# Kernel optimization log

Measured on AMD Instinct MI355X. Metric: run time of the kernel, lower is better.

The kernel has to match this reference:

```python
import jax, jax.numpy as jnp
import numpy as np
from jax import lax

EMB = 128  # embed_length
R = 4      # CBAM reduction


def _mlp(v, w1, b1, w2, b2):
    # shared CAM MLP: [B,C] -> [B,C//r] -> [B,C]
    return jax.nn.relu(v @ w1.T + b1) @ w2.T + b2


def _cbam(x, w1, b1, w2, b2, sw):
    # channel attention (CAM)
    mx = jnp.max(x, axis=(2, 3))
    av = jnp.mean(x, axis=(2, 3))
    gate = jax.nn.sigmoid(_mlp(mx, w1, b1, w2, b2) + _mlp(av, w1, b1, w2, b2))
    y = gate[:, :, None, None] * x
    # spatial attention (SAM): 7x7 conv over [max, mean] channel maps
    smx = jnp.max(y, axis=1, keepdims=True)
    sav = jnp.mean(y, axis=1, keepdims=True)
    s = lax.conv_general_dilated(jnp.concatenate([smx, sav], axis=1), sw,
                                 window_strides=(1, 1), padding=[(3, 3), (3, 3)])
    y = jax.nn.sigmoid(s) * y
    return y + x  # residual as in CBAM.forward


def _neck(x, w, b):
    # 1x1 conv == channel GEMM
    return jnp.einsum('bchw,oc->bohw', x, w) + b[None, :, None, None]


def setup_inputs() -> dict:
    key = jax.random.key(0)
    ks = jax.random.split(key, 40)
    B = 32
    f32 = jnp.float32
    inp = {
        'xin0': jax.random.normal(ks[0], (B, 256, 80, 80), f32),
        'xin1': jax.random.normal(ks[1], (B, 512, 40, 40), f32),
        'xin2': jax.random.normal(ks[2], (B, 1024, 20, 20), f32),
        'yolo_outputs': jax.random.normal(ks[3], (B, 8400, 6), f32),
        'reid_idx': jax.random.randint(ks[4], (B, 100), 0, 8400, dtype=jnp.int32),
        # 1x1 neck convs
        'nw0': jax.random.normal(ks[5], (EMB, 256), f32) * 0.05,
        'nb0': jnp.zeros((EMB,), f32),
        'nw1': jax.random.normal(ks[6], (EMB, 512), f32) * 0.05,
        'nb1': jnp.zeros((EMB,), f32),
        'nw2': jax.random.normal(ks[7], (EMB, 1024), f32) * 0.05,
        'nb2': jnp.zeros((EMB,), f32),
    }
    h = EMB // R
    for i in range(3):
        k = jax.random.split(ks[10 + i], 5)
        inp[f'c{i}w1'] = jax.random.normal(k[0], (h, EMB), f32) * 0.05
        inp[f'c{i}b1'] = jnp.zeros((h,), f32)
        inp[f'c{i}w2'] = jax.random.normal(k[1], (EMB, h), f32) * 0.05
        inp[f'c{i}b2'] = jnp.zeros((EMB,), f32)
        inp[f'c{i}sw'] = jax.random.normal(k[2], (1, 2, 7, 7), f32) * 0.05
    return inp


def reference(xin0, xin1, xin2, yolo_outputs, reid_idx,
              nw0, nb0, nw1, nb1, nw2, nb2,
              c0w1, c0b1, c0w2, c0b2, c0sw,
              c1w1, c1b1, c1w2, c1b2, c1sw,
              c2w1, c2b1, c2w2, c2b2, c2sw):
    f0 = _cbam(_neck(xin0, nw0, nb0), c0w1, c0b1, c0w2, c0b2, c0sw)
    f1 = _cbam(_neck(xin1, nw1, nb1), c1w1, c1b1, c1w2, c1b2, c1sw)
    f2 = _cbam(_neck(xin2, nw2, nb2), c2w1, c2b1, c2w2, c2b2, c2sw)
    B, C = f0.shape[0], f0.shape[1]
    reid_feat = jnp.concatenate([f0.reshape(B, C, -1),
                                 f1.reshape(B, C, -1),
                                 f2.reshape(B, C, -1)], axis=2)  # [B, C, 8400]
    # ragged per-batch gather reid_feat[b, :, reid_idx[b]] then stack columns -> [B*K, C]
    emb = jax.vmap(lambda f, idx: f[:, idx].T)(reid_feat, reid_idx)  # [B, K, C]
    return (yolo_outputs, emb.reshape(-1, C))
```

## Files before the change

### kernel.cpp

```cpp
#include <hip/hip_runtime.h>
#include <hip/hip_bf16.h>

typedef __attribute__((ext_vector_type(8))) short bf16x8;
typedef __attribute__((ext_vector_type(4))) float f32x4;

#define EMB 128
#define NB 32

__device__ __forceinline__ unsigned short f2bf(float f) {
  unsigned u = __float_as_uint(f);
  u = u + 0x7FFFu + ((u >> 16) & 1u);
  return (unsigned short)(u >> 16);
}
__device__ __forceinline__ unsigned ordf(float f) {
  unsigned u = __float_as_uint(f);
  return (u & 0x80000000u) ? ~u : (u | 0x80000000u);
}
__device__ __forceinline__ float unordf(unsigned v) {
  unsigned u = (v & 0x80000000u) ? (v & 0x7FFFFFFFu) : ~v;
  return __uint_as_float(u);
}

__global__ __launch_bounds__(256) void neck_kernel(
    const float* __restrict__ x, const float* __restrict__ w, const float* __restrict__ bias,
    unsigned short* __restrict__ f, unsigned* __restrict__ gmax, float* __restrict__ gsum,
    int K, int HW)
{
  __shared__ unsigned smax[EMB];
  __shared__ float ssum[EMB];
  const int tid = threadIdx.x;
  if (tid < EMB) { smax[tid] = 0u; ssum[tid] = 0.f; }
  __syncthreads();

  const int wv = tid >> 6, lane = tid & 63, q = lane >> 4, col = lane & 15;
  const int b = blockIdx.y;
  const int p0 = blockIdx.x * 128 + wv * 32;
  const float* __restrict__ xb = x + (size_t)b * K * HW;

  f32x4 acc[2][8];
#pragma unroll
  for (int mt = 0; mt < 2; mt++)
#pragma unroll
    for (int nt = 0; nt < 8; nt++) acc[mt][nt] = (f32x4){0.f, 0.f, 0.f, 0.f};

  const int pm0 = min(p0 + col, HW - 1);
  const int pm1 = min(p0 + 16 + col, HW - 1);

  for (int c0 = 0; c0 < K; c0 += 32) {
    const int cb = c0 + q * 8;
    float a0[8], a1[8];
#pragma unroll
    for (int j = 0; j < 8; j++) {
      const float* row = xb + (size_t)(cb + j) * HW;
      a0[j] = row[pm0];
      a1[j] = row[pm1];
    }
    bf16x8 A0, A1;
#pragma unroll
    for (int j = 0; j < 8; j++) { A0[j] = (short)f2bf(a0[j]); A1[j] = (short)f2bf(a1[j]); }
#pragma unroll
    for (int nt = 0; nt < 8; nt++) {
      const float* wr = w + (size_t)(nt * 16 + col) * K + cb;
      const float4 wa = *(const float4*)(wr);
      const float4 wb = *(const float4*)(wr + 4);
      bf16x8 Bf;
      Bf[0] = (short)f2bf(wa.x); Bf[1] = (short)f2bf(wa.y);
      Bf[2] = (short)f2bf(wa.z); Bf[3] = (short)f2bf(wa.w);
      Bf[4] = (short)f2bf(wb.x); Bf[5] = (short)f2bf(wb.y);
      Bf[6] = (short)f2bf(wb.z); Bf[7] = (short)f2bf(wb.w);
      acc[0][nt] = __builtin_amdgcn_mfma_f32_16x16x32_bf16(A0, Bf, acc[0][nt], 0, 0, 0);
      acc[1][nt] = __builtin_amdgcn_mfma_f32_16x16x32_bf16(A1, Bf, acc[1][nt], 0, 0, 0);
    }
  }

#pragma unroll
  for (int nt = 0; nt < 8; nt++) {
    const int o = nt * 16 + col;
    const float bo = bias[o];
    float lmax = -3.4e38f, lsum = 0.f;
#pragma unroll
    for (int mt = 0; mt < 2; mt++) {
#pragma unroll
      for (int r = 0; r < 4; r++) {
        const int p = p0 + mt * 16 + q * 4 + r;
        const float v = acc[mt][nt][r] + bo;
        if (p < HW) {
          f[((size_t)b * HW + p) * EMB + o] = f2bf(v);
          lmax = fmaxf(lmax, v);
          lsum += v;
        }
      }
    }
#pragma unroll
    for (int off = 16; off < 64; off <<= 1) {
      lmax = fmaxf(lmax, __shfl_xor(lmax, off, 64));
      lsum += __shfl_xor(lsum, off, 64);
    }
    if (lane < 16) {
      atomicMax(&smax[o], ordf(lmax));
      atomicAdd(&ssum[o], lsum);
    }
  }
  __syncthreads();
  if (tid < EMB) {
    atomicMax(&gmax[b * EMB + tid], smax[tid]);
    atomicAdd(&gsum[b * EMB + tid], ssum[tid]);
  }
}

__global__ __launch_bounds__(128) void gate_kernel(
    const unsigned* __restrict__ gmax, const float* __restrict__ gsum, float* __restrict__ gate,
    const float* __restrict__ w1a, const float* __restrict__ b1a, const float* __restrict__ w2a, const float* __restrict__ b2a,
    const float* __restrict__ w1b, const float* __restrict__ b1b, const float* __restrict__ w2b, const float* __restrict__ b2b,
    const float* __restrict__ w1c, const float* __restrict__ b1c, const float* __restrict__ w2c, const float* __restrict__ b2c)
{
  const int s = blockIdx.y, b = blockIdx.x, tid = threadIdx.x;
  const float* w1 = s == 0 ? w1a : (s == 1 ? w1b : w1c);
  const float* b1 = s == 0 ? b1a : (s == 1 ? b1b : b1c);
  const float* w2 = s == 0 ? w2a : (s == 1 ? w2b : w2c);
  const float* b2 = s == 0 ? b2a : (s == 1 ? b2b : b2c);
  const float invHW = s == 0 ? (1.f / 6400.f) : (s == 1 ? (1.f / 1600.f) : (1.f / 400.f));
  __shared__ float mx[EMB], av[EMB], hm[32], ha[32];
  const int base = (s * NB + b) * EMB;
  mx[tid] = unordf(gmax[base + tid]);
  av[tid] = gsum[base + tid] * invHW;
  __syncthreads();
  if (tid < 32) {
    float sm = b1[tid], sa = b1[tid];
    for (int c = 0; c < EMB; c++) { const float wv = w1[tid * EMB + c]; sm += wv * mx[c]; sa += wv * av[c]; }
    hm[tid] = fmaxf(sm, 0.f); ha[tid] = fmaxf(sa, 0.f);
  }
  __syncthreads();
  float v = 2.f * b2[tid];
  for (int h = 0; h < 32; h++) { const float wv = w2[tid * 32 + h]; v += wv * (hm[h] + ha[h]); }
  gate[base + tid] = 1.f / (1.f + __expf(-v));
}

__global__ __launch_bounds__(256) void smap_kernel(
    const unsigned short* __restrict__ f0, const unsigned short* __restrict__ f1, const unsigned short* __restrict__ f2,
    const float* __restrict__ gate,
    float* __restrict__ smx0, float* __restrict__ sav0,
    float* __restrict__ smx1, float* __restrict__ sav1,
    float* __restrict__ smx2, float* __restrict__ sav2)
{
  const int lane = threadIdx.x & 63;
  const int wid = (blockIdx.x * blockDim.x + threadIdx.x) >> 6;
  const int nw = (gridDim.x * blockDim.x) >> 6;
  const int total = NB * 8400;
  for (int t = wid; t < total; t += nw) {
    const int b = t / 8400, p = t % 8400;
    const unsigned short* f; float* smx; float* sav; int s, pp, HW;
    if (p < 6400)      { s = 0; pp = p;        HW = 6400; f = f0; smx = smx0; sav = sav0; }
    else if (p < 8000) { s = 1; pp = p - 6400; HW = 1600; f = f1; smx = smx1; sav = sav1; }
    else               { s = 2; pp = p - 8000; HW = 400;  f = f2; smx = smx2; sav = sav2; }
    const unsigned u = ((const unsigned*)(f + ((size_t)b * HW + pp) * EMB))[lane];
    const float v0 = __uint_as_float(u << 16);
    const float v1 = __uint_as_float(u & 0xFFFF0000u);
    const int gb = (s * NB + b) * EMB + 2 * lane;
    const float y0 = gate[gb] * v0, y1 = gate[gb + 1] * v1;
    float m = fmaxf(y0, y1), sm = y0 + y1;
#pragma unroll
    for (int off = 1; off < 64; off <<= 1) { m = fmaxf(m, __shfl_xor(m, off, 64)); sm += __shfl_xor(sm, off, 64); }
    if (lane == 0) { smx[b * HW + pp] = m; sav[b * HW + pp] = sm * (1.f / EMB); }
  }
}

__global__ __launch_bounds__(256) void gather_kernel(
    const int* __restrict__ reid_idx,
    const unsigned short* __restrict__ f0, const unsigned short* __restrict__ f1, const unsigned short* __restrict__ f2,
    const float* __restrict__ gate,
    const float* __restrict__ smx0, const float* __restrict__ sav0,
    const float* __restrict__ smx1, const float* __restrict__ sav1,
    const float* __restrict__ smx2, const float* __restrict__ sav2,
    const float* __restrict__ sw0, const float* __restrict__ sw1, const float* __restrict__ sw2,
    float* __restrict__ emb)
{
  const int lane = threadIdx.x & 63;
  const int wid = (blockIdx.x * blockDim.x + threadIdx.x) >> 6;
  if (wid >= NB * 100) return;
  const int b = wid / 100, k = wid % 100;
  const int idx = reid_idx[b * 100 + k];
  const unsigned short* f; const float* smx; const float* sav; const float* sw;
  int s, pp, W, H, HW;
  if (idx < 6400)      { s = 0; pp = idx;        W = 80; H = 80; HW = 6400; f = f0; smx = smx0; sav = sav0; sw = sw0; }
  else if (idx < 8000) { s = 1; pp = idx - 6400; W = 40; H = 40; HW = 1600; f = f1; smx = smx1; sav = sav1; sw = sw1; }
  else                 { s = 2; pp = idx - 8000; W = 20; H = 20; HW = 400;  f = f2; smx = smx2; sav = sav2; sw = sw2; }
  const int y = pp / W, xx0 = pp % W;
  float c = 0.f;
  if (lane < 49) {
    const int dy = lane / 7 - 3, dx = lane % 7 - 3;
    const int yy = y + dy, xx = xx0 + dx;
    if (yy >= 0 && yy < H && xx >= 0 && xx < W) {
      const int qq = b * HW + yy * W + xx;
      c = smx[qq] * sw[lane] + sav[qq] * sw[49 + lane];
    }
  }
#pragma unroll
  for (int off = 1; off < 64; off <<= 1) c += __shfl_xor(c, off, 64);
  const float sig = 1.f / (1.f + __expf(-c));
  const unsigned u = ((const unsigned*)(f + ((size_t)b * HW + pp) * EMB))[lane];
  const float v0 = __uint_as_float(u << 16);
  const float v1 = __uint_as_float(u & 0xFFFF0000u);
  const int gb = (s * NB + b) * EMB + 2 * lane;
  const float o0 = v0 * (1.f + sig * gate[gb]);
  const float o1 = v1 * (1.f + sig * gate[gb + 1]);
  *(float2*)(emb + ((size_t)(b * 100 + k)) * EMB + 2 * lane) = make_float2(o0, o1);
}

extern "C" void kernel_launch(void* const* d_in, const int* in_sizes, int n_in,
                              void* d_out, int out_size, void* d_ws, size_t ws_size,
                              hipStream_t stream)
{
  const float* xin0 = (const float*)d_in[0];
  const float* xin1 = (const float*)d_in[1];
  const float* xin2 = (const float*)d_in[2];
  const float* yolo = (const float*)d_in[3];
  const int*   reid = (const int*)d_in[4];
  const float* nw0 = (const float*)d_in[5];  const float* nb0 = (const float*)d_in[6];
  const float* nw1 = (const float*)d_in[7];  const float* nb1 = (const float*)d_in[8];
  const float* nw2 = (const float*)d_in[9];  const float* nb2 = (const float*)d_in[10];
  const float* c0w1 = (const float*)d_in[11]; const float* c0b1 = (const float*)d_in[12];
  const float* c0w2 = (const float*)d_in[13]; const float* c0b2 = (const float*)d_in[14];
  const float* c0sw = (const float*)d_in[15];
  const float* c1w1 = (const float*)d_in[16]; const float* c1b1 = (const float*)d_in[17];
  const float* c1w2 = (const float*)d_in[18]; const float* c1b2 = (const float*)d_in[19];
  const float* c1sw = (const float*)d_in[20];
  const float* c2w1 = (const float*)d_in[21]; const float* c2b1 = (const float*)d_in[22];
  const float* c2w2 = (const float*)d_in[23]; const float* c2b2 = (const float*)d_in[24];
  const float* c2sw = (const float*)d_in[25];

  char* ws = (char*)d_ws;
  size_t off = 0;
  auto alloc = [&](size_t bytes) -> void* {
    void* p = ws + off; off += (bytes + 255) & ~(size_t)255; return p;
  };
  unsigned short* f0 = (unsigned short*)alloc((size_t)NB * 6400 * EMB * 2);
  unsigned short* f1 = (unsigned short*)alloc((size_t)NB * 1600 * EMB * 2);
  unsigned short* f2 = (unsigned short*)alloc((size_t)NB * 400 * EMB * 2);
  unsigned* gmax = (unsigned*)alloc(3 * NB * EMB * 4);
  float* gsum = (float*)alloc(3 * NB * EMB * 4);
  float* gate = (float*)alloc(3 * NB * EMB * 4);
  float* smx0 = (float*)alloc((size_t)NB * 6400 * 4);
  float* sav0 = (float*)alloc((size_t)NB * 6400 * 4);
  float* smx1 = (float*)alloc((size_t)NB * 1600 * 4);
  float* sav1 = (float*)alloc((size_t)NB * 1600 * 4);
  float* smx2 = (float*)alloc((size_t)NB * 400 * 4);
  float* sav2 = (float*)alloc((size_t)NB * 400 * 4);

  hipMemsetAsync(gmax, 0, (size_t)2 * 3 * NB * EMB * 4, stream);
  hipMemcpyAsync(d_out, yolo, (size_t)NB * 8400 * 6 * 4, hipMemcpyDeviceToDevice, stream);

  dim3 blk(256);
  neck_kernel<<<dim3(50, NB), blk, 0, stream>>>(xin0, nw0, nb0, f0, gmax + 0 * NB * EMB, gsum + 0 * NB * EMB, 256, 6400);
  neck_kernel<<<dim3(13, NB), blk, 0, stream>>>(xin1, nw1, nb1, f1, gmax + 1 * NB * EMB, gsum + 1 * NB * EMB, 512, 1600);
  neck_kernel<<<dim3(4,  NB), blk, 0, stream>>>(xin2, nw2, nb2, f2, gmax + 2 * NB * EMB, gsum + 2 * NB * EMB, 1024, 400);

  gate_kernel<<<dim3(NB, 3), dim3(128), 0, stream>>>(gmax, gsum, gate,
      c0w1, c0b1, c0w2, c0b2, c1w1, c1b1, c1w2, c1b2, c2w1, c2b1, c2w2, c2b2);

  smap_kernel<<<dim3(4200), blk, 0, stream>>>(f0, f1, f2, gate, smx0, sav0, smx1, sav1, smx2, sav2);

  gather_kernel<<<dim3(800), blk, 0, stream>>>(reid, f0, f1, f2, gate,
      smx0, sav0, smx1, sav1, smx2, sav2, c0sw, c1sw, c2sw,
      (float*)d_out + (size_t)NB * 8400 * 6);
}
```

Before: 710.0 us.

## Stage neck input tiles via LDS, pre-convert weights to bf16, merge launches

Adds a small kernel that converts the neck weights to bf16 once, so the GEMM loop no longer reconverts fp32 weights per block. The input activations are now loaded as coalesced 16-byte global-to-LDS transfers in 64-channel chunks instead of scalar strided loads per lane. The three pyramid-level neck launches are fused into one grid, with the large-K level blocks scheduled first and occupancy hinted at 3. This adds LDS use and two barriers per K chunk, plus an extra tiny kernel launch.

```diff
diff --git a/kernel.cpp b/kernel.cpp
--- a/kernel.cpp
+++ b/kernel.cpp
@@ -20,22 +20,48 @@
   unsigned u = (v & 0x80000000u) ? (v & 0x7FFFFFFFu) : ~v;
   return __uint_as_float(u);
 }
-
-__global__ __launch_bounds__(256) void neck_kernel(
-    const float* __restrict__ x, const float* __restrict__ w, const float* __restrict__ bias,
-    unsigned short* __restrict__ f, unsigned* __restrict__ gmax, float* __restrict__ gsum,
-    int K, int HW)
-{
+__device__ __forceinline__ void gl_lds16(const float* g, float* l) {
+  __builtin_amdgcn_global_load_lds(
+      (const __attribute__((address_space(1))) void*)g,
+      (__attribute__((address_space(3))) void*)l, 16, 0, 0);
+}
+
+__global__ __launch_bounds__(256) void wconv_kernel(
+    const float* __restrict__ w0, const float* __restrict__ w1, const float* __restrict__ w2,
+    unsigned short* __restrict__ o0, unsigned short* __restrict__ o1, unsigned short* __restrict__ o2)
+{
+  const int t = blockIdx.x * 256 + threadIdx.x;
+  const float* w; unsigned short* o; int i;
+  if (t < 32768)       { w = w0; o = o0; i = t; }
+  else if (t < 98304)  { w = w1; o = o1; i = t - 32768; }
+  else                 { w = w2; o = o2; i = t - 98304; }
+  o[i] = f2bf(w[i]);
+}
+
+__global__ __launch_bounds__(256, 3) void neck_kernel(
+    const float* __restrict__ x0, const float* __restrict__ x1, const float* __restrict__ x2,
+    const unsigned short* __restrict__ wb0, const unsigned short* __restrict__ wb1, const unsigned short* __restrict__ wb2,
+    const float* __restrict__ bias0, const float* __restrict__ bias1, const float* __restrict__ bias2,
+    unsigned short* __restrict__ f0o, unsigned short* __restrict__ f1o, unsigned short* __restrict__ f2o,
+    unsigned* __restrict__ gmax, float* __restrict__ gsum)
+{
+  __shared__ float xs[64 * 128];
   __shared__ unsigned smax[EMB];
   __shared__ float ssum[EMB];
   const int tid = threadIdx.x;
   if (tid < EMB) { smax[tid] = 0u; ssum[tid] = 0.f; }
-  __syncthreads();
-
+
+  const int bid = blockIdx.x;
+  int sidx, r, K, HW;
+  const float* x; const unsigned short* wb; const float* bias; unsigned short* f;
+  if (bid < 128)      { sidx = 2; r = bid;       x = x2; wb = wb2; bias = bias2; f = f2o; K = 1024; HW = 400;  }
+  else if (bid < 544) { sidx = 1; r = bid - 128; x = x1; wb = wb1; bias = bias1; f = f1o; K = 512;  HW = 1600; }
+  else                { sidx = 0; r = bid - 544; x = x0; wb = wb0; bias = bias0; f = f0o; K = 256;  HW = 6400; }
+  const int tile = r / NB, b = r % NB;
+  const int p0 = tile * 128;
   const int wv = tid >> 6, lane = tid & 63, q = lane >> 4, col = lane & 15;
-  const int b = blockIdx.y;
-  const int p0 = blockIdx.x * 128 + wv * 32;
   const float* __restrict__ xb = x + (size_t)b * K * HW;
+  const int pw = p0 + wv * 32;
 
   f32x4 acc[2][8];
 #pragma unroll
@@ -43,34 +69,38 @@
 #pragma unroll
     for (int nt = 0; nt < 8; nt++) acc[mt][nt] = (f32x4){0.f, 0.f, 0.f, 0.f};
 
-  const int pm0 = min(p0 + col, HW - 1);
-  const int pm1 = min(p0 + 16 + col, HW - 1);
-
-  for (int c0 = 0; c0 < K; c0 += 32) {
-    const int cb = c0 + q * 8;
-    float a0[8], a1[8];
-#pragma unroll
-    for (int j = 0; j < 8; j++) {
-      const float* row = xb + (size_t)(cb + j) * HW;
-      a0[j] = row[pm0];
-      a1[j] = row[pm1];
-    }
-    bf16x8 A0, A1;
-#pragma unroll
-    for (int j = 0; j < 8; j++) { A0[j] = (short)f2bf(a0[j]); A1[j] = (short)f2bf(a1[j]); }
-#pragma unroll
-    for (int nt = 0; nt < 8; nt++) {
-      const float* wr = w + (size_t)(nt * 16 + col) * K + cb;
-      const float4 wa = *(const float4*)(wr);
-      const float4 wb = *(const float4*)(wr + 4);
-      bf16x8 Bf;
-      Bf[0] = (short)f2bf(wa.x); Bf[1] = (short)f2bf(wa.y);
-      Bf[2] = (short)f2bf(wa.z); Bf[3] = (short)f2bf(wa.w);
-      Bf[4] = (short)f2bf(wb.x); Bf[5] = (short)f2bf(wb.y);
-      Bf[6] = (short)f2bf(wb.z); Bf[7] = (short)f2bf(wb.w);
-      acc[0][nt] = __builtin_amdgcn_mfma_f32_16x16x32_bf16(A0, Bf, acc[0][nt], 0, 0, 0);
-      acc[1][nt] = __builtin_amdgcn_mfma_f32_16x16x32_bf16(A1, Bf, acc[1][nt], 0, 0, 0);
-    }
+  const int pofs = min(p0 + (lane & 31) * 4, HW - 4);
+  const int lrow = lane >> 5;
+
+  for (int k0 = 0; k0 < K; k0 += 64) {
+    const float* gp0 = xb + (size_t)(k0 + wv * 16 + lrow) * HW + pofs;
+    float* lp0 = &xs[(wv * 16) * 128];
+#pragma unroll
+    for (int i = 0; i < 8; i++)
+      gl_lds16(gp0 + (size_t)(2 * i) * HW, lp0 + (2 * i) * 128);
+    __syncthreads();
+
+#pragma unroll
+    for (int kk = 0; kk < 2; kk++) {
+      const int rb = kk * 32 + q * 8;
+      float av0[8], av1[8];
+#pragma unroll
+      for (int j = 0; j < 8; j++) {
+        av0[j] = xs[(rb + j) * 128 + (wv * 32) + col];
+        av1[j] = xs[(rb + j) * 128 + (wv * 32) + 16 + col];
+      }
+      bf16x8 A0, A1;
+#pragma unroll
+      for (int j = 0; j < 8; j++) { A0[j] = (short)f2bf(av0[j]); A1[j] = (short)f2bf(av1[j]); }
+      const int cg = k0 + rb;
+#pragma unroll
+      for (int nt = 0; nt < 8; nt++) {
+        const bf16x8 B = *(const bf16x8*)(wb + (size_t)(nt * 16 + col) * K + cg);
+        acc[0][nt] = __builtin_amdgcn_mfma_f32_16x16x32_bf16(A0, B, acc[0][nt], 0, 0, 0);
+        acc[1][nt] = __builtin_amdgcn_mfma_f32_16x16x32_bf16(A1, B, acc[1][nt], 0, 0, 0);
+      }
+    }
+    __syncthreads();
   }
 
 #pragma unroll
@@ -81,9 +111,9 @@
 #pragma unroll
     for (int mt = 0; mt < 2; mt++) {
 #pragma unroll
-      for (int r = 0; r < 4; r++) {
-        const int p = p0 + mt * 16 + q * 4 + r;
-        const float v = acc[mt][nt][r] + bo;
+      for (int rr = 0; rr < 4; rr++) {
+        const int p = pw + mt * 16 + q * 4 + rr;
+        const float v = acc[mt][nt][rr] + bo;
         if (p < HW) {
           f[((size_t)b * HW + p) * EMB + o] = f2bf(v);
           lmax = fmaxf(lmax, v);
@@ -103,8 +133,8 @@
   }
   __syncthreads();
   if (tid < EMB) {
-    atomicMax(&gmax[b * EMB + tid], smax[tid]);
-    atomicAdd(&gsum[b * EMB + tid], ssum[tid]);
+    atomicMax(&gmax[(sidx * NB + b) * EMB + tid], smax[tid]);
+    atomicAdd(&gsum[(sidx * NB + b) * EMB + tid], ssum[tid]);
   }
 }
 
@@ -246,21 +276,24 @@
   float* sav1 = (float*)alloc((size_t)NB * 1600 * 4);
   float* smx2 = (float*)alloc((size_t)NB * 400 * 4);
   float* sav2 = (float*)alloc((size_t)NB * 400 * 4);
+  unsigned short* wb0 = (unsigned short*)alloc(32768 * 2);
+  unsigned short* wb1 = (unsigned short*)alloc(65536 * 2);
+  unsigned short* wb2 = (unsigned short*)alloc(131072 * 2);
 
   hipMemsetAsync(gmax, 0, (size_t)2 * 3 * NB * EMB * 4, stream);
   hipMemcpyAsync(d_out, yolo, (size_t)NB * 8400 * 6 * 4, hipMemcpyDeviceToDevice, stream);
 
-  dim3 blk(256);
-  neck_kernel<<<dim3(50, NB), blk, 0, stream>>>(xin0, nw0, nb0, f0, gmax + 0 * NB * EMB, gsum + 0 * NB * EMB, 256, 6400);
-  neck_kernel<<<dim3(13, NB), blk, 0, stream>>>(xin1, nw1, nb1, f1, gmax + 1 * NB * EMB, gsum + 1 * NB * EMB, 512, 1600);
-  neck_kernel<<<dim3(4,  NB), blk, 0, stream>>>(xin2, nw2, nb2, f2, gmax + 2 * NB * EMB, gsum + 2 * NB * EMB, 1024, 400);
+  wconv_kernel<<<dim3(896), dim3(256), 0, stream>>>(nw0, nw1, nw2, wb0, wb1, wb2);
+
+  neck_kernel<<<dim3(2144), dim3(256), 0, stream>>>(
+      xin0, xin1, xin2, wb0, wb1, wb2, nb0, nb1, nb2, f0, f1, f2, gmax, gsum);
 
   gate_kernel<<<dim3(NB, 3), dim3(128), 0, stream>>>(gmax, gsum, gate,
       c0w1, c0b1, c0w2, c0b2, c1w1, c1b1, c1w2, c1b2, c2w1, c2b1, c2w2, c2b2);
 
-  smap_kernel<<<dim3(4200), blk, 0, stream>>>(f0, f1, f2, gate, smx0, sav0, smx1, sav1, smx2, sav2);
-
-  gather_kernel<<<dim3(800), blk, 0, stream>>>(reid, f0, f1, f2, gate,
+  smap_kernel<<<dim3(4200), dim3(256), 0, stream>>>(f0, f1, f2, gate, smx0, sav0, smx1, sav1, smx2, sav2);
+
+  gather_kernel<<<dim3(800), dim3(256), 0, stream>>>(reid, f0, f1, f2, gate,
       smx0, sav0, smx1, sav1, smx2, sav2, c0sw, c1sw, c2sw,
       (float*)d_out + (size_t)NB * 8400 * 6);
 }
```

Result: faster. 581.1 us (-18.2%).
